# Kernel tuning notes

Hardware: AMD Instinct MI355X
Metric: run time of the kernel (lower is better)

Reference implementation:

```python
import jax, jax.numpy as jnp
import numpy as np

N_NODES = 50000
NEG_SLOPE = 0.2  # PyG GATConv default leaky_relu slope


def gat_conv(x, src, dst, W, a_src, a_dst, b):
    """One PyG-style GATConv (concat heads, add_self_loops already applied).
    x: [N, F_in]; W: [H*C, F_in]; a_src/a_dst: [H, C]; b: [H*C]."""
    N = x.shape[0]
    H, C = a_src.shape
    h = (x @ W.T).reshape(N, H, C)                       # [N,H,C]
    alpha_src = jnp.einsum('nhc,hc->nh', h, a_src)       # [N,H]
    alpha_dst = jnp.einsum('nhc,hc->nh', h, a_dst)       # [N,H]
    e = alpha_src[src] + alpha_dst[dst]                  # [E,H]
    e = jax.nn.leaky_relu(e, NEG_SLOPE)
    # segment softmax over incoming edges of each dst node, per head
    m = jax.ops.segment_max(e, dst, num_segments=N)      # [N,H]
    w = jnp.exp(e - m[dst])                              # [E,H]
    s = jax.ops.segment_sum(w, dst, num_segments=N)      # [N,H]
    alpha = w / (s[dst] + 1e-16)                         # [E,H]
    msg = alpha[:, :, None] * h[src]                     # [E,H,C]
    out = jax.ops.segment_sum(msg, dst, num_segments=N)  # [N,H,C]
    return out.reshape(N, H * C) + b


def setup_inputs() -> dict:
    key = jax.random.key(0)
    ks = jax.random.split(key, 8)
    N, E, F_in, H, C, L = N_NODES, 800000, 128, 4, 32, 3
    x = jax.random.normal(ks[0], (N, F_in), dtype=jnp.float32)
    edge_index = jax.random.randint(ks[1], (2, E), 0, N, dtype=jnp.int32)
    Ws = jax.random.normal(ks[2], (L, H * C, F_in), dtype=jnp.float32) * 0.1
    att_src = jax.random.normal(ks[3], (L, H, C), dtype=jnp.float32) * 0.1
    att_dst = jax.random.normal(ks[4], (L, H, C), dtype=jnp.float32) * 0.1
    conv_bias = jnp.zeros((L, H * C), dtype=jnp.float32)
    Wf = jax.random.normal(ks[5], (32, H * C), dtype=jnp.float32) * 0.1
    bf = jnp.zeros((32,), dtype=jnp.float32)
    return {"x": x, "Ws": Ws, "att_src": att_src, "att_dst": att_dst,
            "conv_bias": conv_bias, "Wf": Wf, "bf": bf, "edge_index": edge_index}


def reference(x, Ws, att_src, att_dst, conv_bias, Wf, bf, edge_index):
    N = x.shape[0]
    # PyG GATConv add_self_loops=True (default): append i->i for every node
    loop = jnp.arange(N, dtype=edge_index.dtype)
    src = jnp.concatenate([edge_index[0], loop])
    dst = jnp.concatenate([edge_index[1], loop])
    for l in range(Ws.shape[0]):
        x = gat_conv(x, src, dst, Ws[l], att_src[l], att_dst[l], conv_bias[l])
        x = jax.nn.relu(x)
        # F.dropout(p=0.1, training=False) is identity in eval mode
    return x @ Wf.T + bf
```

## Files before the change

kernel.cpp:

```cpp
#include <hip/hip_runtime.h>
#include <hip/hip_bf16.h>
#include <math.h>

#define N_NODES 50000
#define NE      800000
#define F       128
#define NHEAD   4
#define NEG     0.2f

#define CAP 64
#define GM 64
#define GGEMM ((N_NODES + GM - 1) / GM)

#define NPART  256
#define ECHUNK ((NE + NPART - 1) / NPART)
#define NBKT   ((N_NODES + 255) / 256)
#define SUBCAP 64

typedef __attribute__((ext_vector_type(8))) short bf16x8;
typedef __attribute__((ext_vector_type(4))) float f32x4;
typedef _Float16 f16x8 __attribute__((ext_vector_type(8)));


__device__ __forceinline__ unsigned short f2bf(float x) {
    unsigned int u = __float_as_uint(x);
    u += 0x7FFFu + ((u >> 16) & 1u);
    return (unsigned short)(u >> 16);
}
__device__ __forceinline__ float bf2f(unsigned short h) {
    return __uint_as_float(((unsigned int)h) << 16);
}
__device__ __forceinline__ void cvt8(float4 a, float4 b, bf16x8* hi, bf16x8* lo) {
    float f[8] = {a.x, a.y, a.z, a.w, b.x, b.y, b.z, b.w};
    bf16x8 h, l;
#pragma unroll
    for (int j = 0; j < 8; j++) {
        unsigned short hu = f2bf(f[j]);
        h[j] = (short)hu;
        l[j] = (short)f2bf(f[j] - bf2f(hu));
    }
    *hi = h; *lo = l;
}
__device__ __forceinline__ void cvt8h(float4 a, float4 b, f16x8* hi, f16x8* lo) {
    float f[8] = {a.x, a.y, a.z, a.w, b.x, b.y, b.z, b.w};
    f16x8 h, l;
#pragma unroll
    for (int j = 0; j < 8; j++) {
        _Float16 hh = (_Float16)f[j];
        h[j] = hh;
        l[j] = (_Float16)(f[j] - (float)hh);
    }
    *hi = h; *lo = l;
}

__device__ __forceinline__ int lds_unit(int m, int q) {
    return 4 * m + (q ^ ((m >> 1) & 3));
}


__global__ __launch_bounds__(256) void k_gemm_part(
        const float* __restrict__ X,
        const float* __restrict__ W,
        const float* __restrict__ a_s,
        const float* __restrict__ a_d,
        _Float16* __restrict__ hout,
        float* __restrict__ asrc,
        float* __restrict__ adst,
        const int* __restrict__ ei,
        unsigned int* __restrict__ bkt,
        int* __restrict__ cnt2) {
    __shared__ short Ah[256 * 8], Al[256 * 8];
    __shared__ short Bh[512 * 8], Bl[512 * 8];
    __shared__ int pcnt[NBKT];
    int tid = threadIdx.x;

    if (blockIdx.x < NPART) {
        int blk = blockIdx.x;
        if (tid < NBKT) pcnt[tid] = 0;
        __syncthreads();
        int start = blk * ECHUNK;
        int end = start + ECHUNK; if (end > NE) end = NE;
        for (int i = start + tid; i < end; i += 256) {
            unsigned s = (unsigned)ei[i];
            unsigned d = (unsigned)ei[NE + i];
            int b = (int)(d >> 8);
            int r = atomicAdd(&pcnt[b], 1);
            if (r < SUBCAP)
                bkt[(size_t)(b * NPART + blk) * SUBCAP + r] = (d << 16) | s;
        }
        __syncthreads();
        if (tid < NBKT) cnt2[tid * NPART + blk] = pcnt[tid];
        return;
    }

    int bm = (blockIdx.x - NPART) * GM;

    int am = tid >> 2, aq = tid & 3;
    int xunit = ((am >> 4) << 6) + lds_unit(am & 15, aq);
    int wj = tid >> 2, wq = tid & 3;
    int wunit = ((wj >> 4) << 6) + lds_unit(wj & 15, wq);

    int lane = tid & 63, wv = tid >> 6;
    int fm = lane & 15, fq = lane >> 4;
    int a_unit = (wv << 6) + lds_unit(fm, fq);
    int b_unit0 = lds_unit(fm, fq);

    f32x4 acc[8];
#pragma unroll
    for (int nt = 0; nt < 8; nt++) acc[nt] = (f32x4){0.f, 0.f, 0.f, 0.f};

    float4 xp0, xp1, wp0, wp1, wp2, wp3;
    int gr = bm + am;
    bool xok = (gr < N_NODES);
    const float* xrow = X + (size_t)gr * F + aq * 8;
    const float* wrow1 = W + (size_t)wj * F + wq * 8;
    const float* wrow2 = W + (size_t)(wj + 64) * F + wq * 8;
    float4 z4 = make_float4(0.f, 0.f, 0.f, 0.f);

    auto load_tile = [&](int k0) {
        xp0 = xok ? *(const float4*)(xrow + k0)     : z4;
        xp1 = xok ? *(const float4*)(xrow + k0 + 4) : z4;
        wp0 = *(const float4*)(wrow1 + k0);
        wp1 = *(const float4*)(wrow1 + k0 + 4);
        wp2 = *(const float4*)(wrow2 + k0);
        wp3 = *(const float4*)(wrow2 + k0 + 4);
    };
    auto store_tile = [&]() {
        bf16x8 hi, lo;
        cvt8(xp0, xp1, &hi, &lo);
        *(bf16x8*)&Ah[xunit * 8] = hi;  *(bf16x8*)&Al[xunit * 8] = lo;
        cvt8(wp0, wp1, &hi, &lo);
        *(bf16x8*)&Bh[wunit * 8] = hi;  *(bf16x8*)&Bl[wunit * 8] = lo;
        cvt8(wp2, wp3, &hi, &lo);
        *(bf16x8*)&Bh[(wunit + 256) * 8] = hi;  *(bf16x8*)&Bl[(wunit + 256) * 8] = lo;
    };

    load_tile(0);
    store_tile();
    __syncthreads();

#pragma unroll
    for (int t = 0; t < 4; t++) {
        if (t < 3) load_tile((t + 1) * 32);
        bf16x8 ah = *(bf16x8*)&Ah[a_unit * 8];
        bf16x8 al = *(bf16x8*)&Al[a_unit * 8];
#pragma unroll
        for (int nt = 0; nt < 8; nt++) {
            int bu = ((nt << 6) + b_unit0) * 8;
            bf16x8 bh = *(bf16x8*)&Bh[bu];
            bf16x8 bl = *(bf16x8*)&Bl[bu];
            acc[nt] = __builtin_amdgcn_mfma_f32_16x16x32_bf16(ah, bh, acc[nt], 0, 0, 0);
            acc[nt] = __builtin_amdgcn_mfma_f32_16x16x32_bf16(ah, bl, acc[nt], 0, 0, 0);
            acc[nt] = __builtin_amdgcn_mfma_f32_16x16x32_bf16(al, bh, acc[nt], 0, 0, 0);
        }
        __syncthreads();
        if (t < 3) { store_tile(); __syncthreads(); }
    }

    float as_v[8], ad_v[8];
#pragma unroll
    for (int nt = 0; nt < 8; nt++) {
        as_v[nt] = a_s[nt * 16 + fm];
        ad_v[nt] = a_d[nt * 16 + fm];
    }
#pragma unroll
    for (int r = 0; r < 4; r++) {
        int n = bm + wv * 16 + fq * 4 + r;
        bool ok = (n < N_NODES);
        if (ok) {
#pragma unroll
            for (int nt = 0; nt < 8; nt++)
                hout[(size_t)n * F + nt * 16 + fm] = (_Float16)acc[nt][r];
        }
        float ps[4], pd[4];
#pragma unroll
        for (int hh = 0; hh < 4; hh++) {
            ps[hh] = acc[2 * hh][r] * as_v[2 * hh] + acc[2 * hh + 1][r] * as_v[2 * hh + 1];
            pd[hh] = acc[2 * hh][r] * ad_v[2 * hh] + acc[2 * hh + 1][r] * ad_v[2 * hh + 1];
        }
#pragma unroll
        for (int s = 1; s < 16; s <<= 1) {
#pragma unroll
            for (int hh = 0; hh < 4; hh++) {
                ps[hh] += __shfl_xor(ps[hh], s);
                pd[hh] += __shfl_xor(pd[hh], s);
            }
        }
        if (ok && fm == 0) {
            *(float4*)&asrc[n * 4] = make_float4(ps[0], ps[1], ps[2], ps[3]);
            *(float4*)&adst[n * 4] = make_float4(pd[0], pd[1], pd[2], pd[3]);
        }
    }
}


__global__ __launch_bounds__(256) void k_place(const unsigned int* __restrict__ bkt,
                                               const int* __restrict__ cnt2,
                                               int* __restrict__ deg,
                                               int* __restrict__ col) {
    __shared__ int cnt[256];
    int b = blockIdx.x;
    int t = threadIdx.x;
    cnt[t] = 0;
    __syncthreads();
    int c = cnt2[b * NPART + t];
    if (c > SUBCAP) c = SUBCAP;
    const unsigned int* seg = bkt + (size_t)(b * NPART + t) * SUBCAP;
    for (int j = 0; j < c; j++) {
        unsigned int e = seg[j];
        int d = (int)(e >> 16), s = (int)(e & 0xFFFFu);
        int r = atomicAdd(&cnt[d & 255], 1);
        if (r < CAP - 1) col[d * CAP + r] = s;
    }
    __syncthreads();
    int node = (b << 8) + t;
    if (node < N_NODES) {
        int r = cnt[t];
        if (r > CAP - 1) r = CAP - 1;
        col[node * CAP + r] = node;
        deg[node] = r + 1;
    }
}


__global__ __launch_bounds__(256) void k_gemm16(const _Float16* __restrict__ X,
                                                const float* __restrict__ W,
                                                const float* __restrict__ a_s,
                                                const float* __restrict__ a_d,
                                                _Float16* __restrict__ hout,
                                                float* __restrict__ asrc,
                                                float* __restrict__ adst) {
    __shared__ _Float16 Ahf[256 * 8];
    __shared__ _Float16 Bhf[512 * 8], Blf[512 * 8];
    int tid = threadIdx.x;
    int bm = blockIdx.x * GM;

    int am = tid >> 2, aq = tid & 3;
    int xunit = ((am >> 4) << 6) + lds_unit(am & 15, aq);
    int wj = tid >> 2, wq = tid & 3;
    int wunit = ((wj >> 4) << 6) + lds_unit(wj & 15, wq);

    int lane = tid & 63, wv = tid >> 6;
    int fm = lane & 15, fq = lane >> 4;
    int a_unit = (wv << 6) + lds_unit(fm, fq);
    int b_unit0 = lds_unit(fm, fq);

    f32x4 acc[8];
#pragma unroll
    for (int nt = 0; nt < 8; nt++) acc[nt] = (f32x4){0.f, 0.f, 0.f, 0.f};

    f16x8 xp;
    float4 wp0, wp1, wp2, wp3;
    int gr = bm + am;
    bool xok = (gr < N_NODES);
    const _Float16* xrow = X + (size_t)gr * F + aq * 8;
    const float* wrow1 = W + (size_t)wj * F + wq * 8;
    const float* wrow2 = W + (size_t)(wj + 64) * F + wq * 8;

    auto load_tile = [&](int k0) {
        f16x8 zz = {0, 0, 0, 0, 0, 0, 0, 0};
        xp = xok ? *(const f16x8*)(xrow + k0) : zz;
        wp0 = *(const float4*)(wrow1 + k0);
        wp1 = *(const float4*)(wrow1 + k0 + 4);
        wp2 = *(const float4*)(wrow2 + k0);
        wp3 = *(const float4*)(wrow2 + k0 + 4);
    };
    auto store_tile = [&]() {
        *(f16x8*)&Ahf[xunit * 8] = xp;
        f16x8 hi, lo;
        cvt8h(wp0, wp1, &hi, &lo);
        *(f16x8*)&Bhf[wunit * 8] = hi;  *(f16x8*)&Blf[wunit * 8] = lo;
        cvt8h(wp2, wp3, &hi, &lo);
        *(f16x8*)&Bhf[(wunit + 256) * 8] = hi;  *(f16x8*)&Blf[(wunit + 256) * 8] = lo;
    };

    load_tile(0);
    store_tile();
    __syncthreads();

#pragma unroll
    for (int t = 0; t < 4; t++) {
        if (t < 3) load_tile((t + 1) * 32);
        f16x8 ah = *(f16x8*)&Ahf[a_unit * 8];
#pragma unroll
        for (int nt = 0; nt < 8; nt++) {
            int bu = ((nt << 6) + b_unit0) * 8;
            f16x8 bh = *(f16x8*)&Bhf[bu];
            f16x8 bl = *(f16x8*)&Blf[bu];
            acc[nt] = __builtin_amdgcn_mfma_f32_16x16x32_f16(ah, bh, acc[nt], 0, 0, 0);
            acc[nt] = __builtin_amdgcn_mfma_f32_16x16x32_f16(ah, bl, acc[nt], 0, 0, 0);
        }
        __syncthreads();
        if (t < 3) { store_tile(); __syncthreads(); }
    }

    float as_v[8], ad_v[8];
#pragma unroll
    for (int nt = 0; nt < 8; nt++) {
        as_v[nt] = a_s[nt * 16 + fm];
        ad_v[nt] = a_d[nt * 16 + fm];
    }
#pragma unroll
    for (int r = 0; r < 4; r++) {
        int n = bm + wv * 16 + fq * 4 + r;
        bool ok = (n < N_NODES);
        if (ok) {
#pragma unroll
            for (int nt = 0; nt < 8; nt++)
                hout[(size_t)n * F + nt * 16 + fm] = (_Float16)acc[nt][r];
        }
        float ps[4], pd[4];
#pragma unroll
        for (int hh = 0; hh < 4; hh++) {
            ps[hh] = acc[2 * hh][r] * as_v[2 * hh] + acc[2 * hh + 1][r] * as_v[2 * hh + 1];
            pd[hh] = acc[2 * hh][r] * ad_v[2 * hh] + acc[2 * hh + 1][r] * ad_v[2 * hh + 1];
        }
#pragma unroll
        for (int s = 1; s < 16; s <<= 1) {
#pragma unroll
            for (int hh = 0; hh < 4; hh++) {
                ps[hh] += __shfl_xor(ps[hh], s);
                pd[hh] += __shfl_xor(pd[hh], s);
            }
        }
        if (ok && fm == 0) {
            *(float4*)&asrc[n * 4] = make_float4(ps[0], ps[1], ps[2], ps[3]);
            *(float4*)&adst[n * 4] = make_float4(pd[0], pd[1], pd[2], pd[3]);
        }
    }
}


#define EPAD 68

__global__ __launch_bounds__(256) void k_aggr(const _Float16* __restrict__ h,
                                              const float* __restrict__ asrc,
                                              const float* __restrict__ adst,
                                              const int* __restrict__ deg,
                                              const int* __restrict__ col,
                                              const float* __restrict__ bias,
                                              _Float16* __restrict__ xout) {
    __shared__ int   scol[4][64];
    __shared__ float swT[4][4 * EPAD];
    int wave = threadIdx.x >> 6;
    int lane = threadIdx.x & 63;
    int n = blockIdx.x * 4 + wave;
    if (n >= N_NODES) return;
    int wl = lane & 15;
    int he = lane >> 4;
    int hc = wl >> 2;
    int cnt = deg[n]; if (cnt > CAP) cnt = CAP;
    int beg = n * CAP;
    float4 ad4 = *(const float4*)&adst[n * 4];

    float s_run = 0.f;
    float acc[8];
#pragma unroll
    for (int j = 0; j < 8; j++) acc[j] = 0.f;

    {
        int sidx = 0;
        float4 w4 = make_float4(0.f, 0.f, 0.f, 0.f);
        if (lane < cnt) {
            sidx = col[beg + lane];
            float4 av = *(const float4*)&asrc[sidx * 4];
            float ex = av.x + ad4.x, ey = av.y + ad4.y,
                  ez = av.z + ad4.z, ew = av.w + ad4.w;
            ex = (ex > 0.f) ? ex : NEG * ex;
            ey = (ey > 0.f) ? ey : NEG * ey;
            ez = (ez > 0.f) ? ez : NEG * ez;
            ew = (ew > 0.f) ? ew : NEG * ew;
            w4.x = __expf(ex); w4.y = __expf(ey);
            w4.z = __expf(ez); w4.w = __expf(ew);
        }
        scol[wave][lane] = sidx;
        swT[wave][0 * EPAD + lane] = w4.x;
        swT[wave][1 * EPAD + lane] = w4.y;
        swT[wave][2 * EPAD + lane] = w4.z;
        swT[wave][3 * EPAD + lane] = w4.w;
        __builtin_amdgcn_sched_barrier(0);
        float4 wv4 = *(float4*)&swT[wave][he * EPAD + wl * 4];
        float S = (wv4.x + wv4.y) + (wv4.z + wv4.w);
#pragma unroll
        for (int s = 1; s < 16; s <<= 1) S += __shfl_xor(S, s);
        s_run += S;
        __builtin_amdgcn_sched_barrier(0);
#pragma unroll 2
        for (int p = 0; p < cnt; p += 4) {
            int ep = p + he;
            int s = scol[wave][ep];
            float wgt = swT[wave][hc * EPAD + ep];
            f16x8 hv = *(const f16x8*)&h[(size_t)s * F + wl * 8];
#pragma unroll
            for (int j = 0; j < 8; j++)
                acc[j] = fmaf(wgt, (float)hv[j], acc[j]);
        }
    }

#pragma unroll
    for (int j = 0; j < 8; j++) {
        acc[j] += __shfl_xor(acc[j], 16);
        acc[j] += __shfl_xor(acc[j], 32);
    }
    float sv = __shfl(s_run, hc * 16);
    float inv = 1.f / (sv + 1e-16f);
    float4 b0 = *(const float4*)&bias[wl * 8];
    float4 b1 = *(const float4*)&bias[wl * 8 + 4];
    float bb[8] = {b0.x, b0.y, b0.z, b0.w, b1.x, b1.y, b1.z, b1.w};
    if (he == 0) {
        f16x8 st;
#pragma unroll
        for (int j = 0; j < 8; j++)
            st[j] = (_Float16)fmaxf(fmaf(acc[j], inv, bb[j]), 0.f);
        *(f16x8*)&xout[(size_t)n * F + wl * 8] = st;
    }
}


#define FCB 128

__global__ __launch_bounds__(256) void k_fc(const _Float16* __restrict__ X,
                                            const float* __restrict__ Wf,
                                            const float* __restrict__ bf,
                                            float* __restrict__ out) {
    __shared__ float WsT[128 * 36];
    __shared__ float XsT[32 * 132];
    int tid = threadIdx.x;
    int bm = blockIdx.x * FCB;

#pragma unroll
    for (int u = 0; u < 16; u++) {
        int idx = tid + 256 * u;
        int o = idx & 31, k = idx >> 5;
        WsT[k * 36 + o] = Wf[o * 128 + k];
    }

    int tx = tid & 7;
    int ty = tid >> 3;
    float acc[4][4];
#pragma unroll
    for (int i = 0; i < 4; i++)
#pragma unroll
        for (int j = 0; j < 4; j++) acc[i][j] = 0.f;

    for (int k0 = 0; k0 < 128; k0 += 32) {
        __syncthreads();
#pragma unroll
        for (int u = 0; u < 2; u++) {
            int idx = tid + 256 * u;
            int nn = idx & 127, c = idx >> 7;
            int gn = bm + nn;
            f16x8 v = {0, 0, 0, 0, 0, 0, 0, 0};
            if (gn < N_NODES) v = *(const f16x8*)&X[(size_t)gn * F + k0 + c * 8];
#pragma unroll
            for (int j = 0; j < 8; j++)
                XsT[(c * 8 + j) * 132 + nn] = (float)v[j];
        }
        __syncthreads();

#pragma unroll
        for (int kk = 0; kk < 32; kk++) {
            float4 xv = *(float4*)&XsT[kk * 132 + ty * 4];
            float4 wv = *(float4*)&WsT[(k0 + kk) * 36 + tx * 4];
            float xs[4] = {xv.x, xv.y, xv.z, xv.w};
            float ws[4] = {wv.x, wv.y, wv.z, wv.w};
#pragma unroll
            for (int i = 0; i < 4; i++)
#pragma unroll
                for (int j = 0; j < 4; j++)
                    acc[i][j] = fmaf(xs[i], ws[j], acc[i][j]);
        }
    }

    float4 bv = *(const float4*)&bf[tx * 4];
#pragma unroll
    for (int i = 0; i < 4; i++) {
        int n = bm + ty * 4 + i;
        if (n < N_NODES) {
            float4 o4 = make_float4(acc[i][0] + bv.x, acc[i][1] + bv.y,
                                    acc[i][2] + bv.z, acc[i][3] + bv.w);
            *(float4*)&out[n * 32 + tx * 4] = o4;
        }
    }
}


extern "C" void kernel_launch(void* const* d_in, const int* in_sizes, int n_in,
                              void* d_out, int out_size, void* d_ws, size_t ws_size,
                              hipStream_t stream) {
    const float* x      = (const float*)d_in[0];
    const float* Ws     = (const float*)d_in[1];
    const float* a_src  = (const float*)d_in[2];
    const float* a_dst  = (const float*)d_in[3];
    const float* cbias  = (const float*)d_in[4];
    const float* Wf     = (const float*)d_in[5];
    const float* bf     = (const float*)d_in[6];
    const int*   ei     = (const int*)d_in[7];
    float* out = (float*)d_out;

    char* p = (char*)d_ws;
    auto carve = [&](size_t bytes) {
        char* r = p;
        p += (bytes + 255) & ~(size_t)255;
        return r;
    };
    _Float16* xA   = (_Float16*)carve((size_t)N_NODES * F * 2);
    _Float16* xB   = (_Float16*)carve((size_t)N_NODES * F * 2);
    _Float16* xC   = (_Float16*)carve((size_t)N_NODES * F * 2);
    _Float16* hbuf = (_Float16*)carve((size_t)N_NODES * F * 2);
    float* asrc = (float*)carve((size_t)N_NODES * NHEAD * 4);
    float* adst = (float*)carve((size_t)N_NODES * NHEAD * 4);
    int* deg    = (int*)carve((size_t)N_NODES * 4);
    int* col    = (int*)carve((size_t)N_NODES * CAP * 4);
    unsigned int* bkt = (unsigned int*)carve((size_t)NBKT * NPART * SUBCAP * 4);
    int* cnt2   = (int*)carve((size_t)NBKT * NPART * 4);

    int gaggr = (N_NODES + 3) / 4;

    k_gemm_part<<<NPART + GGEMM, 256, 0, stream>>>(
        x, Ws, a_src, a_dst, hbuf, asrc, adst, ei, bkt, cnt2);
    k_place<<<NBKT, 256, 0, stream>>>(bkt, cnt2, deg, col);
    k_aggr<<<gaggr, 256, 0, stream>>>(hbuf, asrc, adst, deg, col, cbias, xA);

    k_gemm16<<<GGEMM, 256, 0, stream>>>(xA, Ws + (size_t)F * F, a_src + F, a_dst + F,
                                        hbuf, asrc, adst);
    k_aggr<<<gaggr, 256, 0, stream>>>(hbuf, asrc, adst, deg, col, cbias + F, xB);

    k_gemm16<<<GGEMM, 256, 0, stream>>>(xB, Ws + (size_t)2 * F * F, a_src + 2 * F,
                                        a_dst + 2 * F, hbuf, asrc, adst);
    k_aggr<<<gaggr, 256, 0, stream>>>(hbuf, asrc, adst, deg, col, cbias + 2 * F, xC);

    k_fc<<<(N_NODES + FCB - 1) / FCB, 256, 0, stream>>>(xC, Wf, bf, out);
}
```

Measured before the change: 277.2 us.

## Stage full weight matrix in LDS and keep X fragments in registers for GEMMs

The GEMM kernels now load and split the entire 128x128 weight matrix into hi/lo halves in XOR-swizzled shared memory once per block. Each wave loads its X row fragments straight into registers, which removes the k-tiled double-buffer loop and its per-tile barriers. Block size grows to 512 threads with 128-row tiles, and the aggregation gather loop unroll goes from 2 to 4. The trade-off is 64KB of LDS per block, which lowers occupancy, and every block redoes the weight conversion; the partition blocks also now run with 512 threads.

Result: slower. 283.6 us (+2.3%).

```diff
diff --git a/kernel.cpp b/kernel.cpp
--- a/kernel.cpp
+++ b/kernel.cpp
@@ -9,7 +9,7 @@
 #define NEG     0.2f
 
 #define CAP 64
-#define GM 64
+#define GM 128
 #define GGEMM ((N_NODES + GM - 1) / GM)
 
 #define NPART  256
@@ -41,24 +41,10 @@
     }
     *hi = h; *lo = l;
 }
-__device__ __forceinline__ void cvt8h(float4 a, float4 b, f16x8* hi, f16x8* lo) {
-    float f[8] = {a.x, a.y, a.z, a.w, b.x, b.y, b.z, b.w};
-    f16x8 h, l;
-#pragma unroll
-    for (int j = 0; j < 8; j++) {
-        _Float16 hh = (_Float16)f[j];
-        h[j] = hh;
-        l[j] = (_Float16)(f[j] - (float)hh);
-    }
-    *hi = h; *lo = l;
-}
-
-__device__ __forceinline__ int lds_unit(int m, int q) {
-    return 4 * m + (q ^ ((m >> 1) & 3));
-}
-
-
-__global__ __launch_bounds__(256) void k_gemm_part(
+
+
+
+__global__ __launch_bounds__(512) void k_gemm_part(
         const float* __restrict__ X,
         const float* __restrict__ W,
         const float* __restrict__ a_s,
@@ -69,8 +55,8 @@
         const int* __restrict__ ei,
         unsigned int* __restrict__ bkt,
         int* __restrict__ cnt2) {
-    __shared__ short Ah[256 * 8], Al[256 * 8];
-    __shared__ short Bh[512 * 8], Bl[512 * 8];
+    __shared__ short Wh[F * F];
+    __shared__ short Wl[F * F];
     __shared__ int pcnt[NBKT];
     int tid = threadIdx.x;
 
@@ -80,7 +66,7 @@
         __syncthreads();
         int start = blk * ECHUNK;
         int end = start + ECHUNK; if (end > NE) end = NE;
-        for (int i = start + tid; i < end; i += 256) {
+        for (int i = start + tid; i < end; i += 512) {
             unsigned s = (unsigned)ei[i];
             unsigned d = (unsigned)ei[NE + i];
             int b = (int)(d >> 8);
@@ -95,66 +81,51 @@
 
     int bm = (blockIdx.x - NPART) * GM;
 
-    int am = tid >> 2, aq = tid & 3;
-    int xunit = ((am >> 4) << 6) + lds_unit(am & 15, aq);
-    int wj = tid >> 2, wq = tid & 3;
-    int wunit = ((wj >> 4) << 6) + lds_unit(wj & 15, wq);
-
-    int lane = tid & 63, wv = tid >> 6;
+#pragma unroll
+    for (int u = 0; u < 32; u++) {
+        int idx = tid + 512 * u;
+        int cw = idx >> 7, k = idx & 127;
+        float v = W[idx];
+        unsigned short h = f2bf(v);
+        unsigned short l = f2bf(v - bf2f(h));
+        int byte = ((cw << 8) + (k << 1)) ^ ((cw & 7) << 4);
+        Wh[byte >> 1] = (short)h;
+        Wl[byte >> 1] = (short)l;
+    }
+
+    int lane = tid & 63, w = tid >> 6;
     int fm = lane & 15, fq = lane >> 4;
-    int a_unit = (wv << 6) + lds_unit(fm, fq);
-    int b_unit0 = lds_unit(fm, fq);
+
+    int arow = bm + w * 16 + fm;
+    bool xok = (arow < N_NODES);
+    const float* xrow = X + (size_t)arow * F + fq * 8;
+    float4 z4 = make_float4(0.f, 0.f, 0.f, 0.f);
+    bf16x8 ah[4], al[4];
+#pragma unroll
+    for (int t = 0; t < 4; t++) {
+        float4 xa = xok ? *(const float4*)(xrow + t * 32)     : z4;
+        float4 xb = xok ? *(const float4*)(xrow + t * 32 + 4) : z4;
+        cvt8(xa, xb, &ah[t], &al[t]);
+    }
+
+    __syncthreads();
 
     f32x4 acc[8];
 #pragma unroll
     for (int nt = 0; nt < 8; nt++) acc[nt] = (f32x4){0.f, 0.f, 0.f, 0.f};
 
-    float4 xp0, xp1, wp0, wp1, wp2, wp3;
-    int gr = bm + am;
-    bool xok = (gr < N_NODES);
-    const float* xrow = X + (size_t)gr * F + aq * 8;
-    const float* wrow1 = W + (size_t)wj * F + wq * 8;
-    const float* wrow2 = W + (size_t)(wj + 64) * F + wq * 8;
-    float4 z4 = make_float4(0.f, 0.f, 0.f, 0.f);
-
-    auto load_tile = [&](int k0) {
-        xp0 = xok ? *(const float4*)(xrow + k0)     : z4;
-        xp1 = xok ? *(const float4*)(xrow + k0 + 4) : z4;
-        wp0 = *(const float4*)(wrow1 + k0);
-        wp1 = *(const float4*)(wrow1 + k0 + 4);
-        wp2 = *(const float4*)(wrow2 + k0);
-        wp3 = *(const float4*)(wrow2 + k0 + 4);
-    };
-    auto store_tile = [&]() {
-        bf16x8 hi, lo;
-        cvt8(xp0, xp1, &hi, &lo);
-        *(bf16x8*)&Ah[xunit * 8] = hi;  *(bf16x8*)&Al[xunit * 8] = lo;
-        cvt8(wp0, wp1, &hi, &lo);
-        *(bf16x8*)&Bh[wunit * 8] = hi;  *(bf16x8*)&Bl[wunit * 8] = lo;
-        cvt8(wp2, wp3, &hi, &lo);
-        *(bf16x8*)&Bh[(wunit + 256) * 8] = hi;  *(bf16x8*)&Bl[(wunit + 256) * 8] = lo;
-    };
-
-    load_tile(0);
-    store_tile();
-    __syncthreads();
-
 #pragma unroll
     for (int t = 0; t < 4; t++) {
-        if (t < 3) load_tile((t + 1) * 32);
-        bf16x8 ah = *(bf16x8*)&Ah[a_unit * 8];
-        bf16x8 al = *(bf16x8*)&Al[a_unit * 8];
-#pragma unroll
-        for (int nt = 0; nt < 8; nt++) {
-            int bu = ((nt << 6) + b_unit0) * 8;
-            bf16x8 bh = *(bf16x8*)&Bh[bu];
-            bf16x8 bl = *(bf16x8*)&Bl[bu];
-            acc[nt] = __builtin_amdgcn_mfma_f32_16x16x32_bf16(ah, bh, acc[nt], 0, 0, 0);
-            acc[nt] = __builtin_amdgcn_mfma_f32_16x16x32_bf16(ah, bl, acc[nt], 0, 0, 0);
-            acc[nt] = __builtin_amdgcn_mfma_f32_16x16x32_bf16(al, bh, acc[nt], 0, 0, 0);
-        }
-        __syncthreads();
-        if (t < 3) { store_tile(); __syncthreads(); }
+#pragma unroll
+        for (int ct = 0; ct < 8; ct++) {
+            int cw = ct * 16 + fm;
+            int byte = ((cw << 8) + (t * 64 + fq * 16)) ^ ((fm & 7) << 4);
+            bf16x8 bh = *(bf16x8*)&Wh[byte >> 1];
+            bf16x8 bl = *(bf16x8*)&Wl[byte >> 1];
+            acc[ct] = __builtin_amdgcn_mfma_f32_16x16x32_bf16(ah[t], bh, acc[ct], 0, 0, 0);
+            acc[ct] = __builtin_amdgcn_mfma_f32_16x16x32_bf16(ah[t], bl, acc[ct], 0, 0, 0);
+            acc[ct] = __builtin_amdgcn_mfma_f32_16x16x32_bf16(al[t], bh, acc[ct], 0, 0, 0);
+        }
     }
 
     float as_v[8], ad_v[8];
@@ -165,7 +136,7 @@
     }
 #pragma unroll
     for (int r = 0; r < 4; r++) {
-        int n = bm + wv * 16 + fq * 4 + r;
+        int n = bm + w * 16 + fq * 4 + r;
         bool ok = (n < N_NODES);
         if (ok) {
 #pragma unroll
@@ -223,75 +194,59 @@
 }
 
 
-__global__ __launch_bounds__(256) void k_gemm16(const _Float16* __restrict__ X,
+__global__ __launch_bounds__(512) void k_gemm16(const _Float16* __restrict__ X,
                                                 const float* __restrict__ W,
                                                 const float* __restrict__ a_s,
                                                 const float* __restrict__ a_d,
                                                 _Float16* __restrict__ hout,
                                                 float* __restrict__ asrc,
                                                 float* __restrict__ adst) {
-    __shared__ _Float16 Ahf[256 * 8];
-    __shared__ _Float16 Bhf[512 * 8], Blf[512 * 8];
+    __shared__ _Float16 Wh[F * F];
+    __shared__ _Float16 Wl[F * F];
     int tid = threadIdx.x;
     int bm = blockIdx.x * GM;
 
-    int am = tid >> 2, aq = tid & 3;
-    int xunit = ((am >> 4) << 6) + lds_unit(am & 15, aq);
-    int wj = tid >> 2, wq = tid & 3;
-    int wunit = ((wj >> 4) << 6) + lds_unit(wj & 15, wq);
-
-    int lane = tid & 63, wv = tid >> 6;
+#pragma unroll
+    for (int u = 0; u < 32; u++) {
+        int idx = tid + 512 * u;
+        int cw = idx >> 7, k = idx & 127;
+        float v = W[idx];
+        _Float16 h = (_Float16)v;
+        _Float16 l = (_Float16)(v - (float)h);
+        int byte = ((cw << 8) + (k << 1)) ^ ((cw & 7) << 4);
+        Wh[byte >> 1] = h;
+        Wl[byte >> 1] = l;
+    }
+
+    int lane = tid & 63, w = tid >> 6;
     int fm = lane & 15, fq = lane >> 4;
-    int a_unit = (wv << 6) + lds_unit(fm, fq);
-    int b_unit0 = lds_unit(fm, fq);
+
+    int arow = bm + w * 16 + fm;
+    bool xok = (arow < N_NODES);
+    const _Float16* xrow = X + (size_t)arow * F + fq * 8;
+    f16x8 zz = {0, 0, 0, 0, 0, 0, 0, 0};
+    f16x8 ax[4];
+#pragma unroll
+    for (int t = 0; t < 4; t++)
+        ax[t] = xok ? *(const f16x8*)(xrow + t * 32) : zz;
+
+    __syncthreads();
 
     f32x4 acc[8];
 #pragma unroll
     for (int nt = 0; nt < 8; nt++) acc[nt] = (f32x4){0.f, 0.f, 0.f, 0.f};
 
-    f16x8 xp;
-    float4 wp0, wp1, wp2, wp3;
-    int gr = bm + am;
-    bool xok = (gr < N_NODES);
-    const _Float16* xrow = X + (size_t)gr * F + aq * 8;
-    const float* wrow1 = W + (size_t)wj * F + wq * 8;
-    const float* wrow2 = W + (size_t)(wj + 64) * F + wq * 8;
-
-    auto load_tile = [&](int k0) {
-        f16x8 zz = {0, 0, 0, 0, 0, 0, 0, 0};
-        xp = xok ? *(const f16x8*)(xrow + k0) : zz;
-        wp0 = *(const float4*)(wrow1 + k0);
-        wp1 = *(const float4*)(wrow1 + k0 + 4);
-        wp2 = *(const float4*)(wrow2 + k0);
-        wp3 = *(const float4*)(wrow2 + k0 + 4);
-    };
-    auto store_tile = [&]() {
-        *(f16x8*)&Ahf[xunit * 8] = xp;
-        f16x8 hi, lo;
-        cvt8h(wp0, wp1, &hi, &lo);
-        *(f16x8*)&Bhf[wunit * 8] = hi;  *(f16x8*)&Blf[wunit * 8] = lo;
-        cvt8h(wp2, wp3, &hi, &lo);
-        *(f16x8*)&Bhf[(wunit + 256) * 8] = hi;  *(f16x8*)&Blf[(wunit + 256) * 8] = lo;
-    };
-
-    load_tile(0);
-    store_tile();
-    __syncthreads();
-
 #pragma unroll
     for (int t = 0; t < 4; t++) {
-        if (t < 3) load_tile((t + 1) * 32);
-        f16x8 ah = *(f16x8*)&Ahf[a_unit * 8];
-#pragma unroll
-        for (int nt = 0; nt < 8; nt++) {
-            int bu = ((nt << 6) + b_unit0) * 8;
-            f16x8 bh = *(f16x8*)&Bhf[bu];
-            f16x8 bl = *(f16x8*)&Blf[bu];
-            acc[nt] = __builtin_amdgcn_mfma_f32_16x16x32_f16(ah, bh, acc[nt], 0, 0, 0);
-            acc[nt] = __builtin_amdgcn_mfma_f32_16x16x32_f16(ah, bl, acc[nt], 0, 0, 0);
-        }
-        __syncthreads();
-        if (t < 3) { store_tile(); __syncthreads(); }
+#pragma unroll
+        for (int ct = 0; ct < 8; ct++) {
+            int cw = ct * 16 + fm;
+            int byte = ((cw << 8) + (t * 64 + fq * 16)) ^ ((fm & 7) << 4);
+            f16x8 bh = *(f16x8*)&Wh[byte >> 1];
+            f16x8 bl = *(f16x8*)&Wl[byte >> 1];
+            acc[ct] = __builtin_amdgcn_mfma_f32_16x16x32_f16(ax[t], bh, acc[ct], 0, 0, 0);
+            acc[ct] = __builtin_amdgcn_mfma_f32_16x16x32_f16(ax[t], bl, acc[ct], 0, 0, 0);
+        }
     }
 
     float as_v[8], ad_v[8];
@@ -302,7 +257,7 @@
     }
 #pragma unroll
     for (int r = 0; r < 4; r++) {
-        int n = bm + wv * 16 + fq * 4 + r;
+        int n = bm + w * 16 + fq * 4 + r;
         bool ok = (n < N_NODES);
         if (ok) {
 #pragma unroll
@@ -385,7 +340,7 @@
         for (int s = 1; s < 16; s <<= 1) S += __shfl_xor(S, s);
         s_run += S;
         __builtin_amdgcn_sched_barrier(0);
-#pragma unroll 2
+#pragma unroll 4
         for (int p = 0; p < cnt; p += 4) {
             int ep = p + he;
             int s = scol[wave][ep];
@@ -517,16 +472,16 @@
 
     int gaggr = (N_NODES + 3) / 4;
 
-    k_gemm_part<<<NPART + GGEMM, 256, 0, stream>>>(
+    k_gemm_part<<<NPART + GGEMM, 512, 0, stream>>>(
         x, Ws, a_src, a_dst, hbuf, asrc, adst, ei, bkt, cnt2);
     k_place<<<NBKT, 256, 0, stream>>>(bkt, cnt2, deg, col);
     k_aggr<<<gaggr, 256, 0, stream>>>(hbuf, asrc, adst, deg, col, cbias, xA);
 
-    k_gemm16<<<GGEMM, 256, 0, stream>>>(xA, Ws + (size_t)F * F, a_src + F, a_dst + F,
+    k_gemm16<<<GGEMM, 512, 0, stream>>>(xA, Ws + (size_t)F * F, a_src + F, a_dst + F,
                                         hbuf, asrc, adst);
     k_aggr<<<gaggr, 256, 0, stream>>>(hbuf, asrc, adst, deg, col, cbias + F, xB);
 
-    k_gemm16<<<GGEMM, 256, 0, stream>>>(xB, Ws + (size_t)2 * F * F, a_src + 2 * F,
+    k_gemm16<<<GGEMM, 512, 0, stream>>>(xB, Ws + (size_t)2 * F * F, a_src + 2 * F,
                                         a_dst + 2 * F, hbuf, asrc, adst);
     k_aggr<<<gaggr, 256, 0, stream>>>(hbuf, asrc, adst, deg, col, cbias + 2 * F, xC);
 
```
